# Optimization experiments

Measured on AMD Instinct MI355X. Metric: run time of the kernel, lower is better.

## Reference

```python
import jax, jax.numpy as jnp
import numpy as np

UNITS = 1024
FEAT = 1024
SEQ = 8192


def setup_inputs() -> dict:
    key = jax.random.key(0)
    ks = jax.random.split(key, 8)
    s = 0.05  # keras RandomUniform(-0.05, 0.05) default-style init
    inputs = jax.random.normal(ks[0], (1, SEQ, FEAT), dtype=jnp.float32)
    f = jax.random.normal(ks[1], (SEQ, 1), dtype=jnp.float32)
    # LSTM params, keras gate order [i, f, c, o]
    W = jax.random.uniform(ks[2], (FEAT, 4 * UNITS), minval=-s, maxval=s, dtype=jnp.float32)
    U = jax.random.uniform(ks[3], (UNITS, 4 * UNITS), minval=-s, maxval=s, dtype=jnp.float32)
    b = jax.random.uniform(ks[4], (4 * UNITS,), minval=-s, maxval=s, dtype=jnp.float32)
    # RackioObserverDense(2, tanh)
    Wd = jax.random.uniform(ks[5], (UNITS, 2), minval=-s, maxval=s, dtype=jnp.float32)
    bd = jax.random.uniform(ks[6], (2,), minval=-s, maxval=s, dtype=jnp.float32)
    return {"inputs": inputs, "f": f, "W": W, "U": U, "b": b, "Wd": Wd, "bd": bd}


def _lstm_linear_act(x, W, U, b):
    # keras LSTM with activation=None: candidate and output activation are identity,
    # recurrent_activation is sigmoid. Gate order i, f, c, o.
    S = x.shape[0]
    units = U.shape[0]
    xz = x @ W + b  # precompute input projection for all steps: (S, 4U)

    def step(carry, xz_t):
        h, c = carry
        z = xz_t + h @ U
        zi, zf, zg, zo = jnp.split(z, 4)
        i = jax.nn.sigmoid(zi)
        fg = jax.nn.sigmoid(zf)
        o = jax.nn.sigmoid(zo)
        c = fg * c + i * zg      # candidate activation = identity
        h = o * c                # output activation = identity
        return (h, c), h

    h0 = jnp.zeros((units,), dtype=x.dtype)
    c0 = jnp.zeros((units,), dtype=x.dtype)
    _, hs = jax.lax.scan(step, (h0, c0), xz)  # (S, units)
    return hs


def reference(inputs, f, W, U, b, Wd, bd):
    x = inputs[0]                               # (S, F); batch must be 1
    hs = _lstm_linear_act(x, W, U, b)           # (S, units), return_sequences=True
    norm = jnp.tanh(hs)                         # self.activation
    h_c = jnp.tanh(norm @ Wd + bd)              # (S, 2), dense with tanh
    # Vectorized finite-difference write into H (original: nested scalar .assign loop)
    # H[i, j] = (h_c[0, i] - h_c[1, i]) / (f[1, j] - f[2, j])
    num = (h_c[0, :] - h_c[1, :])[:, None]      # (2, 1)
    den = (f[1, :] - f[2, :])[None, :]          # (1, 1)
    H = num / den                               # (2, 1)
    h_out = h_c[0, :].reshape(2, 1)
    return (h_out, H)
```

## Files before the change

### kernel.cpp

```cpp
#include <hip/hip_runtime.h>
#include <math.h>

#define UNITS 1024
#define FEAT  1024
#define GATES 4096
#define KC    64
#define KROWS 16

#define OFF_P0  0
#define OFF_P1  (KC*GATES)
#define OFF_PU  (2*KC*GATES)
#define OFF_Z0  (3*KC*GATES)
#define OFF_Z1A (OFF_Z0 + GATES)
#define OFF_Z1  (OFF_Z1A + GATES)

__device__ __forceinline__ float sigmoidf(float x) { return 1.0f / (1.0f + expf(-x)); }

__global__ __launch_bounds__(256) void k_xw(const float* __restrict__ x,
                                            const float* __restrict__ W,
                                            float* __restrict__ ws) {
    int bx = blockIdx.x;
    int jt = bx & 3;
    int kc = bx >> 2;
    int j  = jt * 1024 + threadIdx.x * 4;
    int k0 = kc * KROWS;
    float4 a0 = make_float4(0.f, 0.f, 0.f, 0.f);
    float4 a1 = make_float4(0.f, 0.f, 0.f, 0.f);
    const float* wp = W + (size_t)k0 * GATES + j;
#pragma unroll
    for (int kk = 0; kk < KROWS; ++kk) {
        float x0 = x[k0 + kk];
        float x1 = x[FEAT + k0 + kk];
        float4 w = *reinterpret_cast<const float4*>(wp);
        wp += GATES;
        a0.x += x0 * w.x; a0.y += x0 * w.y; a0.z += x0 * w.z; a0.w += x0 * w.w;
        a1.x += x1 * w.x; a1.y += x1 * w.y; a1.z += x1 * w.z; a1.w += x1 * w.w;
    }
    *reinterpret_cast<float4*>(&ws[OFF_P0 + kc * GATES + j]) = a0;
    *reinterpret_cast<float4*>(&ws[OFF_P1 + kc * GATES + j]) = a1;
}

__global__ __launch_bounds__(256) void k_red1(const float* __restrict__ b,
                                              float* __restrict__ ws) {
    int i = blockIdx.x * 256 + threadIdx.x;
    int c = i & (GATES - 1);
    const float* P = ws + (i < GATES ? OFF_P0 : OFF_P1);
    float s = b[c];
#pragma unroll 8
    for (int kc = 0; kc < KC; ++kc) s += P[kc * GATES + c];
    ws[OFF_Z0 + i] = s;
}

__global__ __launch_bounds__(256) void k_hu(const float* __restrict__ U,
                                            float* __restrict__ ws) {
    int bx = blockIdx.x;
    int jt = bx & 3;
    int kc = bx >> 2;
    int j  = jt * 1024 + threadIdx.x * 4;
    int k0 = kc * KROWS;
    __shared__ float h0s[KROWS];
    if (threadIdx.x < KROWS) {
        const float* Z0 = ws + OFF_Z0;
        int k = k0 + threadIdx.x;
        float c0 = sigmoidf(Z0[k]) * Z0[k + 2 * UNITS];
        h0s[threadIdx.x] = sigmoidf(Z0[k + 3 * UNITS]) * c0;
    }
    __syncthreads();
    float4 a = make_float4(0.f, 0.f, 0.f, 0.f);
    const float* up = U + (size_t)k0 * GATES + j;
#pragma unroll
    for (int kk = 0; kk < KROWS; ++kk) {
        float h = h0s[kk];
        float4 w = *reinterpret_cast<const float4*>(up);
        up += GATES;
        a.x += h * w.x; a.y += h * w.y; a.z += h * w.z; a.w += h * w.w;
    }
    *reinterpret_cast<float4*>(&ws[OFF_PU + kc * GATES + j]) = a;
}

__global__ __launch_bounds__(256) void k_red2(float* __restrict__ ws) {
    int c = blockIdx.x * 256 + threadIdx.x;
    float s = ws[OFF_Z1A + c];
    const float* PU = ws + OFF_PU;
#pragma unroll 8
    for (int kc = 0; kc < KC; ++kc) s += PU[kc * GATES + c];
    ws[OFF_Z1 + c] = s;
}

__global__ __launch_bounds__(1024) void k_final(const float* __restrict__ ws,
                                                const float* __restrict__ f,
                                                const float* __restrict__ Wd,
                                                const float* __restrict__ bd,
                                                float* __restrict__ out) {
    int u = threadIdx.x;
    const float* Z0 = ws + OFF_Z0;
    const float* Z1 = ws + OFF_Z1;
    float c0 = sigmoidf(Z0[u]) * Z0[u + 2 * UNITS];
    float h0 = sigmoidf(Z0[u + 3 * UNITS]) * c0;
    float c1 = sigmoidf(Z1[u + UNITS]) * c0 + sigmoidf(Z1[u]) * Z1[u + 2 * UNITS];
    float h1 = sigmoidf(Z1[u + 3 * UNITS]) * c1;

    float n0 = tanhf(h0);
    float n1 = tanhf(h1);
    float w0 = Wd[2 * u + 0];
    float w1 = Wd[2 * u + 1];

    __shared__ float4 red[1024];
    red[u] = make_float4(n0 * w0, n0 * w1, n1 * w0, n1 * w1);
    __syncthreads();
    for (int s = 512; s > 0; s >>= 1) {
        if (u < s) {
            float4 a = red[u];
            float4 b = red[u + s];
            red[u] = make_float4(a.x + b.x, a.y + b.y, a.z + b.z, a.w + b.w);
        }
        __syncthreads();
    }
    if (u == 0) {
        float4 sa = red[0];
        float hc00 = tanhf(sa.x + bd[0]);
        float hc01 = tanhf(sa.y + bd[1]);
        float hc10 = tanhf(sa.z + bd[0]);
        float hc11 = tanhf(sa.w + bd[1]);
        float den = f[1] - f[2];
        out[0] = hc00;
        out[1] = hc01;
        out[2] = (hc00 - hc10) / den;
        out[3] = (hc01 - hc11) / den;
    }
}

extern "C" void kernel_launch(void* const* d_in, const int* in_sizes, int n_in,
                              void* d_out, int out_size, void* d_ws, size_t ws_size,
                              hipStream_t stream) {
    const float* x  = (const float*)d_in[0];
    const float* f  = (const float*)d_in[1];
    const float* W  = (const float*)d_in[2];
    const float* U  = (const float*)d_in[3];
    const float* b  = (const float*)d_in[4];
    const float* Wd = (const float*)d_in[5];
    const float* bd = (const float*)d_in[6];
    float* out = (float*)d_out;
    float* ws  = (float*)d_ws;

    k_xw  <<<256, 256, 0, stream>>>(x, W, ws);
    k_red1<<< 32, 256, 0, stream>>>(b, ws);
    k_hu  <<<256, 256, 0, stream>>>(U, ws);
    k_red2<<< 16, 256, 0, stream>>>(ws);
    k_final<<< 1, 1024, 0, stream>>>(ws, f, Wd, bd, out);
}
```

Before: 114.0 us.

## Fuse first-step reduction into recurrent GEMV and merge reduction kernels

Drops the separate step-0 reduction kernel. Each k_hu block now reduces, from the partial sums, only the 48 step-0 gate columns it needs, while its U tile is preloaded into registers beforehand. The two remaining reductions are merged into one launch, and the final dot product uses wavefront shuffles instead of a shared-memory tree. This removes one launch plus some serialization, at the cost of redundant partial-sum reads across blocks and more register pressure.

```diff
diff --git a/kernel.cpp b/kernel.cpp
--- a/kernel.cpp
+++ b/kernel.cpp
@@ -11,8 +11,7 @@
 #define OFF_P1  (KC*GATES)
 #define OFF_PU  (2*KC*GATES)
 #define OFF_Z0  (3*KC*GATES)
-#define OFF_Z1A (OFF_Z0 + GATES)
-#define OFF_Z1  (OFF_Z1A + GATES)
+#define OFF_Z1  (OFF_Z0 + GATES)
 
 __device__ __forceinline__ float sigmoidf(float x) { return 1.0f / (1.0f + expf(-x)); }
 
@@ -40,51 +39,85 @@
     *reinterpret_cast<float4*>(&ws[OFF_P1 + kc * GATES + j]) = a1;
 }
 
-__global__ __launch_bounds__(256) void k_red1(const float* __restrict__ b,
-                                              float* __restrict__ ws) {
-    int i = blockIdx.x * 256 + threadIdx.x;
-    int c = i & (GATES - 1);
-    const float* P = ws + (i < GATES ? OFF_P0 : OFF_P1);
-    float s = b[c];
-#pragma unroll 8
-    for (int kc = 0; kc < KC; ++kc) s += P[kc * GATES + c];
-    ws[OFF_Z0 + i] = s;
-}
-
 __global__ __launch_bounds__(256) void k_hu(const float* __restrict__ U,
+                                            const float* __restrict__ b,
                                             float* __restrict__ ws) {
     int bx = blockIdx.x;
     int jt = bx & 3;
     int kc = bx >> 2;
-    int j  = jt * 1024 + threadIdx.x * 4;
+    int tid = threadIdx.x;
+    int j  = jt * 1024 + tid * 4;
     int k0 = kc * KROWS;
+
+    float4 ureg[KROWS];
+    {
+        const float* up = U + (size_t)k0 * GATES + j;
+#pragma unroll
+        for (int kk = 0; kk < KROWS; ++kk) {
+            ureg[kk] = *reinterpret_cast<const float4*>(up);
+            up += GATES;
+        }
+    }
+
+    __shared__ float zred[48][4];
+    __shared__ float zcol[48];
     __shared__ float h0s[KROWS];
-    if (threadIdx.x < KROWS) {
-        const float* Z0 = ws + OFF_Z0;
-        int k = k0 + threadIdx.x;
-        float c0 = sigmoidf(Z0[k]) * Z0[k + 2 * UNITS];
-        h0s[threadIdx.x] = sigmoidf(Z0[k + 3 * UNITS]) * c0;
+    if (tid < 192) {
+        int col_idx = tid >> 2;
+        int part    = tid & 3;
+        int sel     = col_idx >> 4;
+        int off     = (sel == 0) ? 0 : (sel == 1 ? 2 * UNITS : 3 * UNITS);
+        int col     = off + k0 + (col_idx & 15);
+        const float* P0 = ws + OFF_P0;
+        float s = 0.f;
+#pragma unroll
+        for (int kcc = part * 16; kcc < part * 16 + 16; ++kcc)
+            s += P0[kcc * GATES + col];
+        zred[col_idx][part] = s;
     }
     __syncthreads();
+    if (tid < 48) {
+        int sel = tid >> 4;
+        int off = (sel == 0) ? 0 : (sel == 1 ? 2 * UNITS : 3 * UNITS);
+        int col = off + k0 + (tid & 15);
+        zcol[tid] = zred[tid][0] + zred[tid][1] + zred[tid][2] + zred[tid][3] + b[col];
+    }
+    __syncthreads();
+    if (tid < KROWS) {
+        float c0 = sigmoidf(zcol[tid]) * zcol[tid + 16];
+        h0s[tid] = sigmoidf(zcol[tid + 32]) * c0;
+    }
+    __syncthreads();
+
     float4 a = make_float4(0.f, 0.f, 0.f, 0.f);
-    const float* up = U + (size_t)k0 * GATES + j;
 #pragma unroll
     for (int kk = 0; kk < KROWS; ++kk) {
         float h = h0s[kk];
-        float4 w = *reinterpret_cast<const float4*>(up);
-        up += GATES;
-        a.x += h * w.x; a.y += h * w.y; a.z += h * w.z; a.w += h * w.w;
+        a.x += h * ureg[kk].x; a.y += h * ureg[kk].y;
+        a.z += h * ureg[kk].z; a.w += h * ureg[kk].w;
     }
     *reinterpret_cast<float4*>(&ws[OFF_PU + kc * GATES + j]) = a;
 }
 
-__global__ __launch_bounds__(256) void k_red2(float* __restrict__ ws) {
-    int c = blockIdx.x * 256 + threadIdx.x;
-    float s = ws[OFF_Z1A + c];
-    const float* PU = ws + OFF_PU;
+__global__ __launch_bounds__(256) void k_red(const float* __restrict__ b,
+                                             float* __restrict__ ws) {
+    int i = blockIdx.x * 256 + threadIdx.x;
+    if (i < GATES) {
+        int c = i;
+        float s = b[c];
+        const float* P1 = ws + OFF_P1;
+        const float* PU = ws + OFF_PU;
 #pragma unroll 8
-    for (int kc = 0; kc < KC; ++kc) s += PU[kc * GATES + c];
-    ws[OFF_Z1 + c] = s;
+        for (int kc = 0; kc < KC; ++kc) s += P1[kc * GATES + c] + PU[kc * GATES + c];
+        ws[OFF_Z1 + c] = s;
+    } else {
+        int c = i - GATES;
+        float s = b[c];
+        const float* P0 = ws + OFF_P0;
+#pragma unroll 8
+        for (int kc = 0; kc < KC; ++kc) s += P0[kc * GATES + c];
+        ws[OFF_Z0 + c] = s;
+    }
 }
 
 __global__ __launch_bounds__(1024) void k_final(const float* __restrict__ ws,
@@ -102,22 +135,27 @@
 
     float n0 = tanhf(h0);
     float n1 = tanhf(h1);
-    float w0 = Wd[2 * u + 0];
-    float w1 = Wd[2 * u + 1];
+    float2 wd = *reinterpret_cast<const float2*>(&Wd[2 * u]);
 
-    __shared__ float4 red[1024];
-    red[u] = make_float4(n0 * w0, n0 * w1, n1 * w0, n1 * w1);
+    float4 v = make_float4(n0 * wd.x, n0 * wd.y, n1 * wd.x, n1 * wd.y);
+#pragma unroll
+    for (int s = 32; s > 0; s >>= 1) {
+        v.x += __shfl_down(v.x, s);
+        v.y += __shfl_down(v.y, s);
+        v.z += __shfl_down(v.z, s);
+        v.w += __shfl_down(v.w, s);
+    }
+    __shared__ float4 wred[16];
+    int wave = u >> 6;
+    if ((u & 63) == 0) wred[wave] = v;
     __syncthreads();
-    for (int s = 512; s > 0; s >>= 1) {
-        if (u < s) {
-            float4 a = red[u];
-            float4 b = red[u + s];
-            red[u] = make_float4(a.x + b.x, a.y + b.y, a.z + b.z, a.w + b.w);
+    if (u == 0) {
+        float4 sa = wred[0];
+#pragma unroll
+        for (int w = 1; w < 16; ++w) {
+            float4 t = wred[w];
+            sa.x += t.x; sa.y += t.y; sa.z += t.z; sa.w += t.w;
         }
-        __syncthreads();
-    }
-    if (u == 0) {
-        float4 sa = red[0];
         float hc00 = tanhf(sa.x + bd[0]);
         float hc01 = tanhf(sa.y + bd[1]);
         float hc10 = tanhf(sa.z + bd[0]);
@@ -143,9 +181,8 @@
     float* out = (float*)d_out;
     float* ws  = (float*)d_ws;
 
-    k_xw  <<<256, 256, 0, stream>>>(x, W, ws);
-    k_red1<<< 32, 256, 0, stream>>>(b, ws);
-    k_hu  <<<256, 256, 0, stream>>>(U, ws);
-    k_red2<<< 16, 256, 0, stream>>>(ws);
-    k_final<<< 1, 1024, 0, stream>>>(ws, f, Wd, bd, out);
+    k_xw   <<<256, 256, 0, stream>>>(x, W, ws);
+    k_hu   <<<256, 256, 0, stream>>>(U, b, ws);
+    k_red  <<< 32, 256, 0, stream>>>(b, ws);
+    k_final<<<  1, 1024, 0, stream>>>(ws, f, Wd, bd, out);
 }
```

After: 110.5 us. 1.03x faster.
